# Kernel optimization log

Measured on AMD Instinct MI355X. Metric: run time of the kernel, lower is better.

Reference implementation:

```python
import jax, jax.numpy as jnp
import numpy as np

BN_EPS = 1e-5


def setup_inputs() -> dict:
    key = jax.random.key(0)
    ks = jax.random.split(key, 10)
    D, N, NDRUG, NTAIL, NREL = 256, 128, 572, 100000, 100
    return {
        "drug_table": jax.random.normal(ks[0], (NDRUG, D), jnp.float32),
        "rela_table": jax.random.normal(ks[1], (NREL, D), jnp.float32),
        "ent_table": jax.random.normal(ks[2], (NTAIL, D), jnp.float32),
        "W1": jax.random.normal(ks[3], (NDRUG, D, D), jnp.float32),
        "b1": jax.random.normal(ks[4], (N, D), jnp.float32),
        "W2": jax.random.normal(ks[5], (NDRUG, D, D), jnp.float32),
        "b2": jax.random.normal(ks[6], (N, D), jnp.float32),
        "lin_w": jax.random.normal(ks[7], (D, 2 * D), jnp.float32) * (1.0 / np.sqrt(2 * D)),
        "lin_b": jnp.zeros((D,), jnp.float32),
        "bn_gamma": jnp.ones((D,), jnp.float32),
        "bn_beta": jnp.zeros((D,), jnp.float32),
        "drug_name": jnp.arange(NDRUG, dtype=jnp.int64) if jax.config.jax_enable_x64 else jnp.arange(NDRUG, dtype=jnp.int32),
        "adj_tail": jax.random.randint(ks[8], (NDRUG, N), 0, NTAIL, jnp.int32),
        "adj_relation": jax.random.randint(ks[9], (NDRUG, N), 0, NREL, jnp.int32),
    }


def reference(drug_table, rela_table, ent_table, W1, b1, W2, b2,
              lin_w, lin_b, bn_gamma, bn_beta,
              drug_name, adj_tail, adj_relation):
    d = drug_table[drug_name]            # (572, D)
    r = rela_table[adj_relation]         # (572, N, D)
    e = ent_table[adj_tail]              # (572, N, D)

    dr = d[:, None, :] * r               # (572, N, D)
    h = jax.nn.relu(jnp.einsum('bnd,bde->bne', dr, W1) + b1)
    h = jnp.einsum('bnd,bde->bne', h, W2) + b2
    score = jax.nn.softmax(jnp.sum(h, axis=-1), axis=1)   # (572, N)
    w_ent = jnp.einsum('bn,bnd->bd', score, e)             # (572, D)

    x = jnp.concatenate([w_ent, d], axis=1)                # (572, 2D)
    y = jax.nn.relu(x @ lin_w.T + lin_b)                   # (572, D)
    # BatchNorm1d in training mode: batch stats, biased variance
    mean = jnp.mean(y, axis=0)
    var = jnp.var(y, axis=0)
    return bn_gamma * (y - mean) * jax.lax.rsqrt(var + BN_EPS) + bn_beta
```

## Files before the change

kernel.cpp:

```cpp
#include <hip/hip_runtime.h>
#include <math.h>

#define DD   256
#define NN   128
#define NB   572
#define NREL 100
#define KS   32
#define NKS  (DD / KS)
#define EH   128
#define RS   72
#define PSS  132
#define LDRUGS 8

typedef _Float16 h8 __attribute__((ext_vector_type(8)));
typedef _Float16 h2 __attribute__((ext_vector_type(2)));
typedef float    f4 __attribute__((ext_vector_type(4)));

__device__ __forceinline__ float4 ld4(const float* p) {
    return *reinterpret_cast<const float4*>(p);
}
__device__ __forceinline__ void split16(float x, _Float16& hi, _Float16& lo) {
    hi = (_Float16)x;
    lo = (_Float16)(x - (float)hi);
}
__device__ __forceinline__ int slot8(int blk, int row, int hilo) {
    return ((2 * blk + hilo + ((row >> 2) & 7)) & 7) * 8;
}

__global__ __launch_bounds__(256)
void sum_rows(const float* __restrict__ W2, const float* __restrict__ b2,
              float* __restrict__ w2s, float* __restrict__ b2s)
{
    const int blk  = blockIdx.x;
    const int tid  = threadIdx.x;
    const int lane = tid & 63;
    const int wv   = tid >> 6;

    if (blk < 2 * NB) {
        const int b = blk >> 1, half = blk & 1;
        const float* src = W2 + (size_t)b * DD * DD + (size_t)half * (DD / 2) * DD;
        float* dst = w2s + (size_t)b * DD + half * (DD / 2);
        for (int r = wv; r < DD / 2; r += 4) {
            float4 v = ld4(&src[r * DD + lane * 4]);
            float s = v.x + v.y + v.z + v.w;
            #pragma unroll
            for (int m = 32; m >= 1; m >>= 1) s += __shfl_xor(s, m, 64);
            if (lane == 0) dst[r] = s;
        }
    } else {
        for (int r = wv; r < NN; r += 4) {
            float4 v = ld4(&b2[r * DD + lane * 4]);
            float s = v.x + v.y + v.z + v.w;
            #pragma unroll
            for (int m = 32; m >= 1; m >>= 1) s += __shfl_xor(s, m, 64);
            if (lane == 0) b2s[r] = s;
        }
    }
}

__global__ __launch_bounds__(512, 4)
void gnn_mm(const float* __restrict__ drug_table,
            const float* __restrict__ rela_table,
            const float* __restrict__ W1,
            const float* __restrict__ b1,
            const int*   __restrict__ drug_name,
            const int*   __restrict__ adj_relation,
            const float* __restrict__ w2s_g,
            float* __restrict__ part)
{
    __shared__ __align__(16) _Float16 AB_l[2 * 128 * RS];
    __shared__ float d_l[DD];
    __shared__ float w2s_l[EH];
    __shared__ int   rel_l[NN], urel_l[NN], head_l[NN], next_l[NN];
    __shared__ int   map_l[NREL];
    __shared__ int   U_l, c0_l;

    _Float16* A_l = AB_l;
    _Float16* B_l = AB_l + 128 * RS;
    float*    Pl  = reinterpret_cast<float*>(AB_l);

    const int bid  = blockIdx.x;
    const int b    = bid >> 1, h = bid & 1;
    const int tid  = threadIdx.x;
    const int lane = tid & 63;
    const int wv   = tid >> 6;
    const int rg   = wv >> 2;
    const int cg   = wv & 3;
    const int r16  = lane & 15;
    const int gb   = lane >> 4;

    if (tid < NN) { rel_l[tid] = adj_relation[b * NN + tid]; head_l[tid] = -1; }
    if (tid < NREL) map_l[tid] = -1;
    if (tid < DD)  d_l[tid] = drug_table[(size_t)drug_name[b] * DD + tid];
    if (tid >= DD && tid < DD + EH)
        w2s_l[tid - DD] = w2s_g[(size_t)b * DD + h * EH + (tid - DD)];
    __syncthreads();
    if (tid < NN) map_l[rel_l[tid]] = 1;
    __syncthreads();

    bool mk = false; int rank = 0, tot = 0;
    if (tid < 128) {
        mk = (tid < NREL) && (map_l[tid] != -1);
        unsigned long long bal = __ballot(mk);
        rank = __popcll(bal & ((1ull << (tid & 63)) - 1));
        tot  = __popcll(bal);
    }
    if (tid < 64) {
        if (mk) { map_l[tid] = rank; urel_l[rank] = tid; }
        if (tid == 0) c0_l = tot;
    }
    __syncthreads();
    if (tid >= 64 && tid < 128) {
        const int base = c0_l;
        if (mk) { map_l[tid] = base + rank; urel_l[base + rank] = tid; }
        if (tid == 64) U_l = base + tot;
    }
    __syncthreads();
    if (tid < NN)
        next_l[tid] = atomicExch(&head_l[map_l[rel_l[tid]]], tid);
    __syncthreads();

    const int U   = U_l;
    const int NRT = (U + 31) >> 5;

    const float* W1b = W1 + (size_t)b * DD * DD;

    {
        const int padrows = NRT * 32 - U;
        h2 z = {(_Float16)0.f, (_Float16)0.f};
        for (int x = tid; x < padrows * 32; x += 512) {
            int r = U + (x >> 5), m = (x & 31) * 2;
            *(h2*)&A_l[r * RS + m] = z;
        }
    }

    const int kp  = tid >> 5;
    const int el  = tid & 31;
    const int sau = tid >> 2;
    const int sab = tid & 3;

    float4 rbA, rbB, raA, raB;

    #define STAGE_LOAD(kt_) {                                                  \
        const int k0_ = (kt_) * KS;                                            \
        rbA = ld4(&W1b[(size_t)(k0_ + 2 * kp) * DD + h * EH + el * 4]);        \
        rbB = ld4(&W1b[(size_t)(k0_ + 2 * kp + 1) * DD + h * EH + el * 4]);    \
        if (sau < U) {                                                         \
            const float* rr = rela_table + (size_t)urel_l[sau] * DD + k0_ + sab * 8;\
            raA = ld4(rr); raB = ld4(rr + 4);                                  \
        }                                                                      \
    }

    #define STAGE_WRITE(kt_) {                                                 \
        const int k0_ = (kt_) * KS;                                            \
        const float da = d_l[k0_ + 2 * kp], db = d_l[k0_ + 2 * kp + 1];        \
        const float va[4] = {rbA.x, rbA.y, rbA.z, rbA.w};                      \
        const float vb[4] = {rbB.x, rbB.y, rbB.z, rbB.w};                      \
        const int wo = (2 * kp) & 7, bk = kp >> 2;                             \
        for (int i = 0; i < 4; ++i) {                                          \
            const int e = el * 4 + i;                                          \
            _Float16 h0, l0, h1, l1;                                           \
            split16(va[i] * da, h0, l0);                                       \
            split16(vb[i] * db, h1, l1);                                       \
            h2 th = {h0, h1}, tl = {l0, l1};                                   \
            *(h2*)&B_l[e * RS + slot8(bk, e, 0) + wo] = th;                    \
            *(h2*)&B_l[e * RS + slot8(bk, e, 1) + wo] = tl;                    \
        }                                                                      \
        if (sau < U) {                                                         \
            const float vr[8] = {raA.x, raA.y, raA.z, raA.w,                   \
                                 raB.x, raB.y, raB.z, raB.w};                  \
            h8 hv, lv;                                                         \
            for (int j = 0; j < 8; ++j) {                                      \
                _Float16 hh, ll;                                               \
                split16(vr[j], hh, ll);                                        \
                hv[j] = hh; lv[j] = ll;                                        \
            }                                                                  \
            *(h8*)&A_l[sau * RS + slot8(sab, sau, 0)] = hv;                    \
            *(h8*)&A_l[sau * RS + slot8(sab, sau, 1)] = lv;                    \
        }                                                                      \
    }

    STAGE_LOAD(0);
    STAGE_WRITE(0);
    __syncthreads();

    f4 acc[2][2][2];
    #pragma unroll
    for (int p = 0; p < 2; ++p)
        #pragma unroll
        for (int sr = 0; sr < 2; ++sr)
            #pragma unroll
            for (int sc = 0; sc < 2; ++sc)
                acc[p][sr][sc] = {0.f, 0.f, 0.f, 0.f};

    for (int kt = 0; kt < NKS; ++kt) {
        if (kt + 1 < NKS) STAGE_LOAD(kt + 1);

        h8 bh[2], bl[2];
        #pragma unroll
        for (int sc = 0; sc < 2; ++sc) {
            const int e = cg * 32 + sc * 16 + r16;
            bh[sc] = *(const h8*)&B_l[e * RS + slot8(gb, e, 0)];
            bl[sc] = *(const h8*)&B_l[e * RS + slot8(gb, e, 1)];
        }
        #pragma unroll
        for (int p = 0; p < 2; ++p) {
            const int rt = rg + 2 * p;
            if (rt < NRT) {
                #pragma unroll
                for (int sr = 0; sr < 2; ++sr) {
                    const int row = rt * 32 + sr * 16 + r16;
                    h8 ah = *(const h8*)&A_l[row * RS + slot8(gb, row, 0)];
                    h8 al = *(const h8*)&A_l[row * RS + slot8(gb, row, 1)];
                    #pragma unroll
                    for (int sc = 0; sc < 2; ++sc) {
                        acc[p][sr][sc] = __builtin_amdgcn_mfma_f32_16x16x32_f16(ah, bh[sc], acc[p][sr][sc], 0, 0, 0);
                        acc[p][sr][sc] = __builtin_amdgcn_mfma_f32_16x16x32_f16(al, bh[sc], acc[p][sr][sc], 0, 0, 0);
                        acc[p][sr][sc] = __builtin_amdgcn_mfma_f32_16x16x32_f16(ah, bl[sc], acc[p][sr][sc], 0, 0, 0);
                    }
                }
            }
        }
        __syncthreads();
        if (kt + 1 < NKS) STAGE_WRITE(kt + 1);
        __syncthreads();
    }
    #undef STAGE_LOAD
    #undef STAGE_WRITE

    const int ug   = tid >> 4;
    const int td16 = tid & 15;
    float4 w0 = ld4(&w2s_l[td16 * 8]);
    float4 w1v = ld4(&w2s_l[td16 * 8 + 4]);

    for (int rt = 0; rt < 4; ++rt) {
        if (rt < NRT) {
            __syncthreads();
            if ((rt & 1) == rg) {
                const int p = rt >> 1;
                #pragma unroll
                for (int sr = 0; sr < 2; ++sr)
                    #pragma unroll
                    for (int sc = 0; sc < 2; ++sc)
                        #pragma unroll
                        for (int jj = 0; jj < 4; ++jj)
                            Pl[(sr * 16 + gb * 4 + jj) * PSS + cg * 32 + sc * 16 + r16] =
                                acc[p][sr][sc][jj];
            }
            __syncthreads();
            const int u = rt * 32 + ug;
            if (u < U) {
                float4 p0 = ld4(&Pl[ug * PSS + td16 * 8]);
                float4 p1 = ld4(&Pl[ug * PSS + td16 * 8 + 4]);
                int n = head_l[u];
                while (n >= 0) {
                    const float* bp = b1 + (size_t)n * DD + h * EH + td16 * 8;
                    float4 b0 = ld4(bp);
                    float4 b1v = ld4(bp + 4);
                    float s = fmaxf(p0.x + b0.x,  0.f) * w0.x
                            + fmaxf(p0.y + b0.y,  0.f) * w0.y
                            + fmaxf(p0.z + b0.z,  0.f) * w0.z
                            + fmaxf(p0.w + b0.w,  0.f) * w0.w
                            + fmaxf(p1.x + b1v.x, 0.f) * w1v.x
                            + fmaxf(p1.y + b1v.y, 0.f) * w1v.y
                            + fmaxf(p1.z + b1v.z, 0.f) * w1v.z
                            + fmaxf(p1.w + b1v.w, 0.f) * w1v.w;
                    #pragma unroll
                    for (int m = 8; m >= 1; m >>= 1) s += __shfl_xor(s, m, 16);
                    if (td16 == 0) part[(size_t)b * 256 + h * NN + n] = s;
                    n = next_l[n];
                }
            }
        }
    }
}

__global__ __launch_bounds__(256)
void gnn_gather(const float* __restrict__ drug_table,
                const float* __restrict__ ent_table,
                const int*   __restrict__ drug_name,
                const int*   __restrict__ adj_tail,
                const float* __restrict__ part,
                const float* __restrict__ b2s_g,
                float* __restrict__ xbuf)
{
    __shared__ float score_l[NN];
    __shared__ int   tail_l[NN];

    const int b = blockIdx.x, tid = threadIdx.x;

    if (tid < NN) {
        tail_l[tid]  = adj_tail[b * NN + tid];
        score_l[tid] = part[(size_t)b * 256 + tid]
                     + part[(size_t)b * 256 + NN + tid] + b2s_g[tid];
    }
    __syncthreads();

    if (tid < 64) {
        float l0 = score_l[tid], l1 = score_l[tid + 64];
        float M = fmaxf(l0, l1);
        #pragma unroll
        for (int m = 32; m >= 1; m >>= 1) M = fmaxf(M, __shfl_xor(M, m, 64));
        float e0 = expf(l0 - M), e1 = expf(l1 - M);
        float S = e0 + e1;
        #pragma unroll
        for (int m = 32; m >= 1; m >>= 1) S += __shfl_xor(S, m, 64);
        float inv = 1.f / S;
        score_l[tid]      = e0 * inv;
        score_l[tid + 64] = e1 * inv;
    }
    __syncthreads();

    float w = 0.f;
    for (int n = 0; n < NN; ++n) {
        float s = score_l[n];
        if (s > 1e-9f)
            w = fmaf(s, ent_table[(size_t)tail_l[n] * DD + tid], w);
    }
    xbuf[(size_t)b * 512 + tid]       = w;
    xbuf[(size_t)b * 512 + 256 + tid] = drug_table[(size_t)drug_name[b] * DD + tid];
}

__global__ __launch_bounds__(256)
void gnn_lin(const float* __restrict__ lin_w,
             const float* __restrict__ lin_b,
             const float* __restrict__ xbuf,
             float* __restrict__ Y)
{
    __shared__ float x_l[LDRUGS * 512];

    const int g = blockIdx.x, tid = threadIdx.x;
    const int b0 = g * LDRUGS;

    #pragma unroll
    for (int i = 0; i < LDRUGS * 2; ++i) {
        int f = tid + i * 256;
        *reinterpret_cast<float4*>(&x_l[f * 4]) = ld4(&xbuf[(size_t)b0 * 512 + f * 4]);
    }
    __syncthreads();

    const float* lw = lin_w + (size_t)tid * 512;
    float dot[LDRUGS];
    #pragma unroll
    for (int d = 0; d < LDRUGS; ++d) dot[d] = 0.f;

    for (int k4 = 0; k4 < 128; ++k4) {
        float4 wv = ld4(&lw[k4 * 4]);
        #pragma unroll
        for (int d = 0; d < LDRUGS; ++d) {
            float4 xv = ld4(&x_l[d * 512 + k4 * 4]);
            dot[d] += wv.x * xv.x + wv.y * xv.y + wv.z * xv.z + wv.w * xv.w;
        }
    }

    const float bb = lin_b[tid];
    #pragma unroll
    for (int d = 0; d < LDRUGS; ++d) {
        if (b0 + d < NB)
            Y[(size_t)(b0 + d) * DD + tid] = fmaxf(dot[d] + bb, 0.f);
    }
}

__global__ void bn_stats(const float* __restrict__ Y, float* __restrict__ stats)
{
    int d = blockIdx.x, t = threadIdx.x;
    float s = 0.f, ss = 0.f;
    for (int b = t; b < NB; b += 64) {
        float v = Y[(size_t)b * DD + d];
        s += v; ss += v * v;
    }
    #pragma unroll
    for (int m = 32; m >= 1; m >>= 1) {
        s  += __shfl_xor(s, m, 64);
        ss += __shfl_xor(ss, m, 64);
    }
    if (t == 0) {
        float mean = s * (1.f / NB);
        float var  = ss * (1.f / NB) - mean * mean;
        stats[d]      = mean;
        stats[DD + d] = rsqrtf(var + 1e-5f);
    }
}

__global__ void bn_apply(float* __restrict__ Y, const float* __restrict__ stats,
                         const float* __restrict__ gamma, const float* __restrict__ beta)
{
    int b = blockIdx.x, t = threadIdx.x;
    float mean = stats[t], inv = stats[DD + t];
    float v = Y[(size_t)b * DD + t];
    Y[(size_t)b * DD + t] = gamma[t] * (v - mean) * inv + beta[t];
}

extern "C" void kernel_launch(void* const* d_in, const int* in_sizes, int n_in,
                              void* d_out, int out_size, void* d_ws, size_t ws_size,
                              hipStream_t stream)
{
    const float* drug_table = (const float*)d_in[0];
    const float* rela_table = (const float*)d_in[1];
    const float* ent_table  = (const float*)d_in[2];
    const float* W1         = (const float*)d_in[3];
    const float* b1         = (const float*)d_in[4];
    const float* W2         = (const float*)d_in[5];
    const float* b2         = (const float*)d_in[6];
    const float* lin_w      = (const float*)d_in[7];
    const float* lin_b      = (const float*)d_in[8];
    const float* bn_g       = (const float*)d_in[9];
    const float* bn_b       = (const float*)d_in[10];
    const int*   drug_name  = (const int*)d_in[11];
    const int*   adj_tail   = (const int*)d_in[12];
    const int*   adj_rel    = (const int*)d_in[13];
    float* out = (float*)d_out;

    const int NBP = ((NB + LDRUGS - 1) / LDRUGS) * LDRUGS;
    float* w2s   = (float*)d_ws;
    float* b2s   = w2s + (size_t)NB * DD;
    float* part  = b2s + NN;
    float* xbuf  = part + (size_t)NB * 256;
    float* stats = xbuf + (size_t)NBP * 512;

    sum_rows<<<2 * NB + 1, 256, 0, stream>>>(W2, b2, w2s, b2s);
    gnn_mm<<<2 * NB, 512, 0, stream>>>(drug_table, rela_table, W1, b1,
                                       drug_name, adj_rel, w2s, part);
    gnn_gather<<<NB, 256, 0, stream>>>(drug_table, ent_table, drug_name,
                                       adj_tail, part, b2s, xbuf);
    gnn_lin<<<NBP / LDRUGS, 256, 0, stream>>>(lin_w, lin_b, xbuf, out);
    bn_stats<<<DD, 64, 0, stream>>>(out, stats);
    bn_apply<<<NB, DD, 0, stream>>>(out, stats, bn_g, bn_b);
}
```

Before: 134.3 us.

## Fuse W2 row-sum into main GEMM loop and rework LDS swizzle

Removes the separate sum_rows kernel and computes each block's W2 row sums inside the GEMM k-loop, overlapping those loads with the MFMA work and avoiding a round trip through global memory for w2s. A small kernel still sums b2. Each thread now loads W1 with strided scalar loads instead of float4, and the LDS row stride and swizzle move to an XOR pattern to cut bank conflicts. The gnn_mm kernel now carries extra global traffic and per-thread shuffle work, and the scalar W1 loads may coalesce less well.

```diff
diff --git a/kernel.cpp b/kernel.cpp
--- a/kernel.cpp
+++ b/kernel.cpp
@@ -8,7 +8,7 @@
 #define KS   32
 #define NKS  (DD / KS)
 #define EH   128
-#define RS   72
+#define RS   80
 #define PSS  132
 #define LDRUGS 8
 
@@ -23,39 +23,18 @@
     hi = (_Float16)x;
     lo = (_Float16)(x - (float)hi);
 }
-__device__ __forceinline__ int slot8(int blk, int row, int hilo) {
-    return ((2 * blk + hilo + ((row >> 2) & 7)) & 7) * 8;
-}
-
-__global__ __launch_bounds__(256)
-void sum_rows(const float* __restrict__ W2, const float* __restrict__ b2,
-              float* __restrict__ w2s, float* __restrict__ b2s)
-{
-    const int blk  = blockIdx.x;
-    const int tid  = threadIdx.x;
-    const int lane = tid & 63;
-    const int wv   = tid >> 6;
-
-    if (blk < 2 * NB) {
-        const int b = blk >> 1, half = blk & 1;
-        const float* src = W2 + (size_t)b * DD * DD + (size_t)half * (DD / 2) * DD;
-        float* dst = w2s + (size_t)b * DD + half * (DD / 2);
-        for (int r = wv; r < DD / 2; r += 4) {
-            float4 v = ld4(&src[r * DD + lane * 4]);
-            float s = v.x + v.y + v.z + v.w;
-            #pragma unroll
-            for (int m = 32; m >= 1; m >>= 1) s += __shfl_xor(s, m, 64);
-            if (lane == 0) dst[r] = s;
-        }
-    } else {
-        for (int r = wv; r < NN; r += 4) {
-            float4 v = ld4(&b2[r * DD + lane * 4]);
-            float s = v.x + v.y + v.z + v.w;
-            #pragma unroll
-            for (int m = 32; m >= 1; m >>= 1) s += __shfl_xor(s, m, 64);
-            if (lane == 0) b2s[r] = s;
-        }
-    }
+__device__ __forceinline__ int slotx(int blk2, int row) {
+    return ((blk2 ^ (row & 7)) & 7) * 8;
+}
+
+__global__ void sum_b2(const float* __restrict__ b2, float* __restrict__ b2s)
+{
+    const int n = blockIdx.x, t = threadIdx.x;
+    float4 v = ld4(&b2[n * DD + t * 4]);
+    float s = v.x + v.y + v.z + v.w;
+    #pragma unroll
+    for (int m = 32; m >= 1; m >>= 1) s += __shfl_xor(s, m, 64);
+    if (t == 0) b2s[n] = s;
 }
 
 __global__ __launch_bounds__(512, 4)
@@ -63,9 +42,9 @@
             const float* __restrict__ rela_table,
             const float* __restrict__ W1,
             const float* __restrict__ b1,
+            const float* __restrict__ W2,
             const int*   __restrict__ drug_name,
             const int*   __restrict__ adj_relation,
-            const float* __restrict__ w2s_g,
             float* __restrict__ part)
 {
     __shared__ __align__(16) _Float16 AB_l[2 * 128 * RS];
@@ -92,8 +71,6 @@
     if (tid < NN) { rel_l[tid] = adj_relation[b * NN + tid]; head_l[tid] = -1; }
     if (tid < NREL) map_l[tid] = -1;
     if (tid < DD)  d_l[tid] = drug_table[(size_t)drug_name[b] * DD + tid];
-    if (tid >= DD && tid < DD + EH)
-        w2s_l[tid - DD] = w2s_g[(size_t)b * DD + h * EH + (tid - DD)];
     __syncthreads();
     if (tid < NN) map_l[rel_l[tid]] = 1;
     __syncthreads();
@@ -124,13 +101,15 @@
     const int NRT = (U + 31) >> 5;
 
     const float* W1b = W1 + (size_t)b * DD * DD;
+    const float* W2b = W2 + (size_t)b * DD * DD;
 
     {
         const int padrows = NRT * 32 - U;
-        h2 z = {(_Float16)0.f, (_Float16)0.f};
-        for (int x = tid; x < padrows * 32; x += 512) {
-            int r = U + (x >> 5), m = (x & 31) * 2;
-            *(h2*)&A_l[r * RS + m] = z;
+        h8 z = {(_Float16)0.f,(_Float16)0.f,(_Float16)0.f,(_Float16)0.f,
+                (_Float16)0.f,(_Float16)0.f,(_Float16)0.f,(_Float16)0.f};
+        for (int x = tid; x < padrows * 8; x += 512) {
+            int r = U + (x >> 3), c = (x & 7) * 8;
+            *(h8*)&A_l[r * RS + c] = z;
         }
     }
 
@@ -139,12 +118,18 @@
     const int sau = tid >> 2;
     const int sab = tid & 3;
 
-    float4 rbA, rbB, raA, raB;
+    float rb0[4], rb1[4];
+    float4 raA, raB;
 
     #define STAGE_LOAD(kt_) {                                                  \
         const int k0_ = (kt_) * KS;                                            \
-        rbA = ld4(&W1b[(size_t)(k0_ + 2 * kp) * DD + h * EH + el * 4]);        \
-        rbB = ld4(&W1b[(size_t)(k0_ + 2 * kp + 1) * DD + h * EH + el * 4]);    \
+        const float* w1p0 = &W1b[(size_t)(k0_ + 2 * kp) * DD + h * EH + el];   \
+        const float* w1p1 = w1p0 + DD;                                         \
+        _Pragma("unroll")                                                      \
+        for (int i = 0; i < 4; ++i) {                                          \
+            rb0[i] = w1p0[32 * i];                                             \
+            rb1[i] = w1p1[32 * i];                                             \
+        }                                                                      \
         if (sau < U) {                                                         \
             const float* rr = rela_table + (size_t)urel_l[sau] * DD + k0_ + sab * 8;\
             raA = ld4(rr); raB = ld4(rr + 4);                                  \
@@ -154,29 +139,30 @@
     #define STAGE_WRITE(kt_) {                                                 \
         const int k0_ = (kt_) * KS;                                            \
         const float da = d_l[k0_ + 2 * kp], db = d_l[k0_ + 2 * kp + 1];        \
-        const float va[4] = {rbA.x, rbA.y, rbA.z, rbA.w};                      \
-        const float vb[4] = {rbB.x, rbB.y, rbB.z, rbB.w};                      \
-        const int wo = (2 * kp) & 7, bk = kp >> 2;                             \
+        const int bk2 = 2 * (kp >> 2);                                         \
+        const int wo  = (2 * kp) & 7;                                          \
+        _Pragma("unroll")                                                      \
         for (int i = 0; i < 4; ++i) {                                          \
-            const int e = el * 4 + i;                                          \
+            const int e = el + 32 * i;                                         \
             _Float16 h0, l0, h1, l1;                                           \
-            split16(va[i] * da, h0, l0);                                       \
-            split16(vb[i] * db, h1, l1);                                       \
+            split16(rb0[i] * da, h0, l0);                                      \
+            split16(rb1[i] * db, h1, l1);                                      \
             h2 th = {h0, h1}, tl = {l0, l1};                                   \
-            *(h2*)&B_l[e * RS + slot8(bk, e, 0) + wo] = th;                    \
-            *(h2*)&B_l[e * RS + slot8(bk, e, 1) + wo] = tl;                    \
+            *(h2*)&B_l[e * RS + slotx(bk2,     e) + wo] = th;                  \
+            *(h2*)&B_l[e * RS + slotx(bk2 + 1, e) + wo] = tl;                  \
         }                                                                      \
         if (sau < U) {                                                         \
             const float vr[8] = {raA.x, raA.y, raA.z, raA.w,                   \
                                  raB.x, raB.y, raB.z, raB.w};                  \
             h8 hv, lv;                                                         \
+            _Pragma("unroll")                                                  \
             for (int j = 0; j < 8; ++j) {                                      \
                 _Float16 hh, ll;                                               \
                 split16(vr[j], hh, ll);                                        \
                 hv[j] = hh; lv[j] = ll;                                        \
             }                                                                  \
-            *(h8*)&A_l[sau * RS + slot8(sab, sau, 0)] = hv;                    \
-            *(h8*)&A_l[sau * RS + slot8(sab, sau, 1)] = lv;                    \
+            *(h8*)&A_l[sau * RS + slotx(2 * sab,     sau)] = hv;               \
+            *(h8*)&A_l[sau * RS + slotx(2 * sab + 1, sau)] = lv;               \
         }                                                                      \
     }
 
@@ -196,12 +182,15 @@
     for (int kt = 0; kt < NKS; ++kt) {
         if (kt + 1 < NKS) STAGE_LOAD(kt + 1);
 
+        float4 rw0 = ld4(&W2b[(size_t)(h * EH + kt * 16 + 2 * wv)     * DD + lane * 4]);
+        float4 rw1 = ld4(&W2b[(size_t)(h * EH + kt * 16 + 2 * wv + 1) * DD + lane * 4]);
+
         h8 bh[2], bl[2];
         #pragma unroll
         for (int sc = 0; sc < 2; ++sc) {
             const int e = cg * 32 + sc * 16 + r16;
-            bh[sc] = *(const h8*)&B_l[e * RS + slot8(gb, e, 0)];
-            bl[sc] = *(const h8*)&B_l[e * RS + slot8(gb, e, 1)];
+            bh[sc] = *(const h8*)&B_l[e * RS + slotx(2 * gb,     e)];
+            bl[sc] = *(const h8*)&B_l[e * RS + slotx(2 * gb + 1, e)];
         }
         #pragma unroll
         for (int p = 0; p < 2; ++p) {
@@ -210,8 +199,8 @@
                 #pragma unroll
                 for (int sr = 0; sr < 2; ++sr) {
                     const int row = rt * 32 + sr * 16 + r16;
-                    h8 ah = *(const h8*)&A_l[row * RS + slot8(gb, row, 0)];
-                    h8 al = *(const h8*)&A_l[row * RS + slot8(gb, row, 1)];
+                    h8 ah = *(const h8*)&A_l[row * RS + slotx(2 * gb,     row)];
+                    h8 al = *(const h8*)&A_l[row * RS + slotx(2 * gb + 1, row)];
                     #pragma unroll
                     for (int sc = 0; sc < 2; ++sc) {
                         acc[p][sr][sc] = __builtin_amdgcn_mfma_f32_16x16x32_f16(ah, bh[sc], acc[p][sr][sc], 0, 0, 0);
@@ -221,6 +210,21 @@
                 }
             }
         }
+
+        {
+            float s0 = rw0.x + rw0.y + rw0.z + rw0.w;
+            float s1 = rw1.x + rw1.y + rw1.z + rw1.w;
+            #pragma unroll
+            for (int m = 32; m >= 1; m >>= 1) {
+                s0 += __shfl_xor(s0, m, 64);
+                s1 += __shfl_xor(s1, m, 64);
+            }
+            if (lane == 0) {
+                w2s_l[kt * 16 + 2 * wv]     = s0;
+                w2s_l[kt * 16 + 2 * wv + 1] = s1;
+            }
+        }
+
         __syncthreads();
         if (kt + 1 < NKS) STAGE_WRITE(kt + 1);
         __syncthreads();
@@ -412,15 +416,14 @@
     float* out = (float*)d_out;
 
     const int NBP = ((NB + LDRUGS - 1) / LDRUGS) * LDRUGS;
-    float* w2s   = (float*)d_ws;
-    float* b2s   = w2s + (size_t)NB * DD;
+    float* b2s   = (float*)d_ws;
     float* part  = b2s + NN;
     float* xbuf  = part + (size_t)NB * 256;
     float* stats = xbuf + (size_t)NBP * 512;
 
-    sum_rows<<<2 * NB + 1, 256, 0, stream>>>(W2, b2, w2s, b2s);
-    gnn_mm<<<2 * NB, 512, 0, stream>>>(drug_table, rela_table, W1, b1,
-                                       drug_name, adj_rel, w2s, part);
+    sum_b2<<<NN, 64, 0, stream>>>(b2, b2s);
+    gnn_mm<<<2 * NB, 512, 0, stream>>>(drug_table, rela_table, W1, b1, W2,
+                                       drug_name, adj_rel, part);
     gnn_gather<<<NB, 256, 0, stream>>>(drug_table, ent_table, drug_name,
                                        adj_tail, part, b2s, xbuf);
     gnn_lin<<<NBP / LDRUGS, 256, 0, stream>>>(lin_w, lin_b, xbuf, out);
```

Result: faster. 130.4 us (-2.9%).
